# Kernel optimization log

Hardware: AMD Instinct MI355X
Metric: run time of the kernel (lower is better)

## Reference

```python
import jax, jax.numpy as jnp
import numpy as np

N_NODES = 50000


def _sage_conv(x, src, dst, Wl, Wr, b):
    """SAGEConv with mean aggregation: lin_l(mean_j x_j) + lin_r(x_i) + b."""
    msgs = x[src]                                                # [E, Din] gather
    agg = jax.ops.segment_sum(msgs, dst, num_segments=N_NODES)  # [N, Din] scatter-add
    cnt = jax.ops.segment_sum(jnp.ones((src.shape[0], 1), x.dtype), dst,
                              num_segments=N_NODES)             # [N, 1]
    agg = agg / jnp.maximum(cnt, 1.0)                           # mean
    return agg @ Wl.T + x @ Wr.T + b                            # [N, Dout]


def setup_inputs() -> dict:
    key = jax.random.key(0)
    ks = jax.random.split(key, 8)
    d_in, d_h = 64, 128
    x = jax.random.normal(ks[0], (N_NODES, d_in), dtype=jnp.float32)
    edge_index = jax.random.randint(ks[1], (2, 800000), 0, N_NODES, dtype=jnp.int32)
    s1 = 1.0 / np.sqrt(d_in)
    s2 = 1.0 / np.sqrt(d_h)
    return {
        "x": x,
        "edge_index": edge_index,
        "Wl1": jax.random.normal(ks[2], (d_h, d_in), dtype=jnp.float32) * s1,
        "Wr1": jax.random.normal(ks[3], (d_h, d_in), dtype=jnp.float32) * s1,
        "b1": jnp.zeros((d_h,), dtype=jnp.float32),
        "Wl2": jax.random.normal(ks[4], (d_h, d_h), dtype=jnp.float32) * s2,
        "Wr2": jax.random.normal(ks[5], (d_h, d_h), dtype=jnp.float32) * s2,
        "b2": jnp.zeros((d_h,), dtype=jnp.float32),
    }


def reference(x, edge_index, Wl1, Wr1, b1, Wl2, Wr2, b2):
    src, dst = edge_index[0], edge_index[1]
    # layer 1: conv -> dropout(eval: identity) -> ReLU
    h = jax.nn.relu(_sage_conv(x, src, dst, Wl1, Wr1, b1))
    # layer 2
    h = jax.nn.relu(_sage_conv(h, src, dst, Wl2, Wr2, b2))
    return h
```

## Files before the change

### kernel.cpp

```cpp
#include <hip/hip_runtime.h>

#define N_NODES 50000
#define NBUCK 391
#define BCAP 4096
#define BSHIFT 12

typedef __attribute__((ext_vector_type(8))) short short8;
typedef __attribute__((ext_vector_type(4))) float floatx4;

static __device__ __forceinline__ unsigned short f2bf(float f) {
  unsigned int u = __builtin_bit_cast(unsigned int, f);
  u += 0x7fff + ((u >> 16) & 1);
  return (unsigned short)(u >> 16);
}
static __device__ __forceinline__ float bf2f(unsigned short s) {
  unsigned int u = ((unsigned int)s) << 16;
  return __builtin_bit_cast(float, u);
}


__global__ void cast_x(const float* __restrict__ x, unsigned short* __restrict__ A1, int total) {
  int i = blockIdx.x * blockDim.x + threadIdx.x;
  if (i >= total) return;
  A1[(size_t)(i >> 6) * 128 + 64 + (i & 63)] = f2bf(x[i]);
}

__global__ void cast_w(const float* __restrict__ Wl1, const float* __restrict__ Wr1,
                       const float* __restrict__ Wl2, const float* __restrict__ Wr2,
                       unsigned short* __restrict__ W1, unsigned short* __restrict__ W2) {
  int t = blockIdx.x * blockDim.x + threadIdx.x;
  if (t < 128 * 128) {
    int c = t >> 7, k = t & 127;
    W1[t] = f2bf(k < 64 ? Wl1[c * 64 + k] : Wr1[c * 64 + k - 64]);
  } else {
    int t2 = t - 128 * 128;
    if (t2 < 128 * 256) {
      int c = t2 >> 8, k = t2 & 255;
      W2[t2] = f2bf(k < 128 ? Wl2[c * 128 + k] : Wr2[c * 128 + k - 128]);
    }
  }
}


__global__ void __launch_bounds__(1024) bucket_scatter(
    const int* __restrict__ src, const int* __restrict__ dst,
    int* __restrict__ bucket_cur, int* __restrict__ buf, int E) {
  __shared__ int hist[NBUCK];
  __shared__ int base_s[NBUCK];
  int t = threadIdx.x;
  for (int i = t; i < NBUCK; i += 1024) hist[i] = 0;
  __syncthreads();
  int e0 = blockIdx.x * 4096;
  int sv[4], dv[4], bv[4];
#pragma unroll
  for (int p = 0; p < 4; ++p) {
    int e = e0 + p * 1024 + t;
    if (e < E) {
      sv[p] = src[e];
      dv[p] = dst[e];
      bv[p] = dv[p] >> 7;
      atomicAdd(&hist[bv[p]], 1);
    } else bv[p] = -1;
  }
  __syncthreads();
  for (int i = t; i < NBUCK; i += 1024) {
    int c = hist[i];
    base_s[i] = c > 0 ? atomicAdd(&bucket_cur[i], c) : 0;
  }
  __syncthreads();
  for (int i = t; i < NBUCK; i += 1024) hist[i] = 0;
  __syncthreads();
#pragma unroll
  for (int p = 0; p < 4; ++p) {
    if (bv[p] >= 0) {
      int sub = base_s[bv[p]] + atomicAdd(&hist[bv[p]], 1);
      if (sub < BCAP) buf[(bv[p] << BSHIFT) + sub] = (sv[p] << 7) | (dv[p] & 127);
    }
  }
}

__global__ void __launch_bounds__(256) bucket_csr(
    int* __restrict__ buf, const int* __restrict__ bucket_cur,
    int* __restrict__ row_start, int* __restrict__ row_cnt, int n) {
  __shared__ int eb[BCAP];
  __shared__ int cnt[128];
  __shared__ int tmp[128];
  __shared__ int cur[128];
  const int t = threadIdx.x;
  const int b = blockIdx.x;
  const int node0 = b << 7;
  const int len = min(bucket_cur[b], BCAP);
  int* reg = buf + (b << BSHIFT);
  if (t < 128) cnt[t] = 0;
  __syncthreads();
  for (int i = t; i < len; i += 256) {
    int p = reg[i];
    eb[i] = p;
    atomicAdd(&cnt[p & 127], 1);
  }
  __syncthreads();
  if (t < 128) tmp[t] = cnt[t];
  __syncthreads();
#pragma unroll
  for (int off = 1; off < 128; off <<= 1) {
    int u = (t >= off && t < 128) ? tmp[t - off] : 0;
    __syncthreads();
    if (t < 128) tmp[t] += u;
    __syncthreads();
  }
  if (t < 128) {
    int ex = tmp[t] - cnt[t];
    cur[t] = ex;
    int nd = node0 + t;
    if (nd < n) {
      row_start[nd] = (b << BSHIFT) + ex;
      row_cnt[nd] = cnt[t];
    }
  }
  __syncthreads();
  for (int i = t; i < len; i += 256) {
    int p = eb[i];
    int sub = atomicAdd(&cur[p & 127], 1);
    reg[sub] = p >> 7;
  }
}


__global__ void agg_mean64(unsigned short* __restrict__ A1,
    const int* __restrict__ row_start, const int* __restrict__ row_cnt,
    const int* __restrict__ srcs, int n) {
  int wid = (blockIdx.x * blockDim.x + threadIdx.x) >> 6;
  int lane = threadIdx.x & 63;
  if (wid >= n) return;
  int start = row_start[wid];
  int cnt = row_cnt[wid];
  float a0 = 0.f, a1 = 0.f, a2 = 0.f, a3 = 0.f;
  int e = 0;
  for (; e + 4 <= cnt; e += 4) {
    int s0 = srcs[start + e];
    int s1 = srcs[start + e + 1];
    int s2 = srcs[start + e + 2];
    int s3 = srcs[start + e + 3];
    a0 += bf2f(A1[(size_t)s0 * 128 + 64 + lane]);
    a1 += bf2f(A1[(size_t)s1 * 128 + 64 + lane]);
    a2 += bf2f(A1[(size_t)s2 * 128 + 64 + lane]);
    a3 += bf2f(A1[(size_t)s3 * 128 + 64 + lane]);
  }
  for (; e < cnt; ++e) a0 += bf2f(A1[(size_t)srcs[start + e] * 128 + 64 + lane]);
  A1[(size_t)wid * 128 + lane] = f2bf((a0 + a1 + a2 + a3) * (1.0f / (float)max(cnt, 1)));
}

__global__ void agg_mean128(unsigned short* __restrict__ A2,
    const int* __restrict__ row_start, const int* __restrict__ row_cnt,
    const int* __restrict__ srcs, int n) {
  int wid = (blockIdx.x * blockDim.x + threadIdx.x) >> 6;
  int lane = threadIdx.x & 63;
  if (wid >= n) return;
  int start = row_start[wid];
  int cnt = row_cnt[wid];
  float ax = 0.f, ay = 0.f, bx = 0.f, by = 0.f;
  float cx = 0.f, cy = 0.f, dx = 0.f, dy = 0.f;
  int e = 0;
  for (; e + 4 <= cnt; e += 4) {
    int s0 = srcs[start + e];
    int s1 = srcs[start + e + 1];
    int s2 = srcs[start + e + 2];
    int s3 = srcs[start + e + 3];
    unsigned int u0 = *(const unsigned int*)(A2 + (size_t)s0 * 256 + 128 + lane * 2);
    unsigned int u1 = *(const unsigned int*)(A2 + (size_t)s1 * 256 + 128 + lane * 2);
    unsigned int u2 = *(const unsigned int*)(A2 + (size_t)s2 * 256 + 128 + lane * 2);
    unsigned int u3 = *(const unsigned int*)(A2 + (size_t)s3 * 256 + 128 + lane * 2);
    ax += bf2f((unsigned short)u0); ay += bf2f((unsigned short)(u0 >> 16));
    bx += bf2f((unsigned short)u1); by += bf2f((unsigned short)(u1 >> 16));
    cx += bf2f((unsigned short)u2); cy += bf2f((unsigned short)(u2 >> 16));
    dx += bf2f((unsigned short)u3); dy += bf2f((unsigned short)(u3 >> 16));
  }
  for (; e < cnt; ++e) {
    unsigned int u0 = *(const unsigned int*)(A2 + (size_t)srcs[start + e] * 256 + 128 + lane * 2);
    ax += bf2f((unsigned short)u0); ay += bf2f((unsigned short)(u0 >> 16));
  }
  float inv = 1.0f / (float)max(cnt, 1);
  unsigned int packed = (unsigned int)f2bf((ax + bx + cx + dx) * inv)
                      | ((unsigned int)f2bf((ay + by + cy + dy) * inv) << 16);
  *(unsigned int*)(A2 + (size_t)wid * 256 + lane * 2) = packed;
}


template<int KP, bool BF_OUT>
__global__ void __launch_bounds__(256) mfma_gemm(
    const unsigned short* __restrict__ A, const unsigned short* __restrict__ W,
    const float* __restrict__ bias, unsigned short* __restrict__ outb,
    float* __restrict__ outf, int n, int ostride, int ocol) {
  const int lane = threadIdx.x & 63;
  const int wv = threadIdx.x >> 6;
  const int m = lane & 15;
  const int q = lane >> 4;
  const int r0 = blockIdx.x * 128 + wv * 32;

  floatx4 acc[2][8];
#pragma unroll
  for (int rt = 0; rt < 2; ++rt)
#pragma unroll
    for (int ct = 0; ct < 8; ++ct) acc[rt][ct] = (floatx4){0.f, 0.f, 0.f, 0.f};

  int ra = r0 + m;      if (ra > n - 1) ra = n - 1;
  int rb = r0 + 16 + m; if (rb > n - 1) rb = n - 1;
  const unsigned short* Arow0 = A + (size_t)ra * KP + q * 8;
  const unsigned short* Arow1 = A + (size_t)rb * KP + q * 8;
  const unsigned short* Wrow  = W + (size_t)m * KP + q * 8;

#pragma unroll 1
  for (int kc = 0; kc < KP / 32; ++kc) {
    short8 a0 = *(const short8*)(Arow0 + kc * 32);
    short8 a1 = *(const short8*)(Arow1 + kc * 32);
#pragma unroll
    for (int ct = 0; ct < 8; ++ct) {
      short8 wf = *(const short8*)(Wrow + (size_t)ct * 16 * KP + kc * 32);
      acc[0][ct] = __builtin_amdgcn_mfma_f32_16x16x32_bf16(a0, wf, acc[0][ct], 0, 0, 0);
      acc[1][ct] = __builtin_amdgcn_mfma_f32_16x16x32_bf16(a1, wf, acc[1][ct], 0, 0, 0);
    }
  }

  float bv[8];
#pragma unroll
  for (int ct = 0; ct < 8; ++ct) bv[ct] = bias[ct * 16 + m];

#pragma unroll
  for (int rt = 0; rt < 2; ++rt) {
#pragma unroll
    for (int j = 0; j < 4; ++j) {
      int row = r0 + rt * 16 + q * 4 + j;
      if (row < n) {
#pragma unroll
        for (int ct = 0; ct < 8; ++ct) {
          float v = acc[rt][ct][j] + bv[ct];
          v = v > 0.f ? v : 0.f;
          int col = ct * 16 + m;
          if (BF_OUT) outb[(size_t)row * ostride + ocol + col] = f2bf(v);
          else        outf[(size_t)row * ostride + col] = v;
        }
      }
    }
  }
}


extern "C" void kernel_launch(void* const* d_in, const int* in_sizes, int n_in,
                              void* d_out, int out_size, void* d_ws, size_t ws_size,
                              hipStream_t stream) {
  const int N = N_NODES;
  const int E = in_sizes[1] / 2;
  const float* x   = (const float*)d_in[0];
  const int*   src = (const int*)d_in[1];
  const int*   dst = src + E;
  const float* Wl1 = (const float*)d_in[2];
  const float* Wr1 = (const float*)d_in[3];
  const float* b1  = (const float*)d_in[4];
  const float* Wl2 = (const float*)d_in[5];
  const float* Wr2 = (const float*)d_in[6];
  const float* b2  = (const float*)d_in[7];
  float* out = (float*)d_out;

  unsigned short* A1 = (unsigned short*)d_ws;
  unsigned short* A2 = A1 + (size_t)N * 128;
  unsigned short* W1 = A2 + (size_t)N * 256;
  unsigned short* W2 = W1 + 128 * 128;
  int* row_start  = (int*)(W2 + 128 * 256);
  int* row_cnt    = row_start + N;
  int* bucket_cur = row_cnt + N;
  int* buf        = bucket_cur + 392;

  hipMemsetAsync(bucket_cur, 0, NBUCK * sizeof(int), stream);
  cast_x<<<(N * 64 + 255) / 256, 256, 0, stream>>>(x, A1, N * 64);
  cast_w<<<(128 * 128 + 128 * 256 + 255) / 256, 256, 0, stream>>>(Wl1, Wr1, Wl2, Wr2, W1, W2);

  bucket_scatter<<<(E + 4095) / 4096, 1024, 0, stream>>>(src, dst, bucket_cur, buf, E);
  bucket_csr<<<NBUCK, 256, 0, stream>>>(buf, bucket_cur, row_start, row_cnt, N);

  int ab = (N * 64 + 255) / 256;
  agg_mean64<<<ab, 256, 0, stream>>>(A1, row_start, row_cnt, buf, N);

  int gb = (N + 127) / 128;
  mfma_gemm<128, true><<<gb, 256, 0, stream>>>(A1, W1, b1, A2, nullptr, N, 256, 128);

  agg_mean128<<<ab, 256, 0, stream>>>(A2, row_start, row_cnt, buf, N);
  mfma_gemm<256, false><<<gb, 256, 0, stream>>>(A2, W2, b2, nullptr, out, N, 128, 0);
}
```

Before: 215.3 us.

## Fuse prep casts and memset into one kernel; fuse CSR build with layer-1 aggregation

The x cast, weight casts and bucket counter memset are merged into a single grid-stride prep kernel, removing two launches and a memset. The per-bucket CSR builder now runs with 1024 threads and, after building its 128 node rows, does the layer-1 mean aggregation for those nodes directly from shared counts. This drops a separate aggregation launch and its row_start/row_cnt reads. The trade-off is lower parallelism: 391 blocks, each with 16 waves covering 128 nodes. The prep kernel also uses a fixed 512-block grid.

```diff
diff --git a/kernel.cpp b/kernel.cpp
--- a/kernel.cpp
+++ b/kernel.cpp
@@ -19,26 +19,25 @@
 }
 
 
-__global__ void cast_x(const float* __restrict__ x, unsigned short* __restrict__ A1, int total) {
-  int i = blockIdx.x * blockDim.x + threadIdx.x;
-  if (i >= total) return;
-  A1[(size_t)(i >> 6) * 128 + 64 + (i & 63)] = f2bf(x[i]);
-}
-
-__global__ void cast_w(const float* __restrict__ Wl1, const float* __restrict__ Wr1,
-                       const float* __restrict__ Wl2, const float* __restrict__ Wr2,
-                       unsigned short* __restrict__ W1, unsigned short* __restrict__ W2) {
-  int t = blockIdx.x * blockDim.x + threadIdx.x;
-  if (t < 128 * 128) {
-    int c = t >> 7, k = t & 127;
-    W1[t] = f2bf(k < 64 ? Wl1[c * 64 + k] : Wr1[c * 64 + k - 64]);
-  } else {
-    int t2 = t - 128 * 128;
-    if (t2 < 128 * 256) {
-      int c = t2 >> 8, k = t2 & 255;
-      W2[t2] = f2bf(k < 128 ? Wl2[c * 128 + k] : Wr2[c * 128 + k - 128]);
-    }
-  }
+__global__ void __launch_bounds__(256) prep(
+    const float* __restrict__ x,
+    const float* __restrict__ Wl1, const float* __restrict__ Wr1,
+    const float* __restrict__ Wl2, const float* __restrict__ Wr2,
+    unsigned short* __restrict__ A1, unsigned short* __restrict__ W1,
+    unsigned short* __restrict__ W2, int* __restrict__ bucket_cur, int n) {
+  const int gid = blockIdx.x * 256 + threadIdx.x;
+  const int gsz = gridDim.x * 256;
+  for (int i = gid; i < n * 64; i += gsz)
+    A1[(size_t)(i >> 6) * 128 + 64 + (i & 63)] = f2bf(x[i]);
+  for (int i = gid; i < 128 * 128; i += gsz) {
+    int c = i >> 7, k = i & 127;
+    W1[i] = f2bf(k < 64 ? Wl1[c * 64 + k] : Wr1[c * 64 + k - 64]);
+  }
+  for (int i = gid; i < 128 * 256; i += gsz) {
+    int c = i >> 8, k = i & 255;
+    W2[i] = f2bf(k < 128 ? Wl2[c * 128 + k] : Wr2[c * 128 + k - 128]);
+  }
+  for (int i = gid; i < NBUCK; i += gsz) bucket_cur[i] = 0;
 }
 
 
@@ -79,9 +78,11 @@
   }
 }
 
-__global__ void __launch_bounds__(256) bucket_csr(
+
+__global__ void __launch_bounds__(1024) bucket_csr_agg64(
     int* __restrict__ buf, const int* __restrict__ bucket_cur,
-    int* __restrict__ row_start, int* __restrict__ row_cnt, int n) {
+    int* __restrict__ row_start, int* __restrict__ row_cnt,
+    unsigned short* __restrict__ A1, int n) {
   __shared__ int eb[BCAP];
   __shared__ int cnt[128];
   __shared__ int tmp[128];
@@ -93,7 +94,7 @@
   int* reg = buf + (b << BSHIFT);
   if (t < 128) cnt[t] = 0;
   __syncthreads();
-  for (int i = t; i < len; i += 256) {
+  for (int i = t; i < len; i += 1024) {
     int p = reg[i];
     eb[i] = p;
     atomicAdd(&cnt[p & 127], 1);
@@ -118,37 +119,36 @@
     }
   }
   __syncthreads();
-  for (int i = t; i < len; i += 256) {
+  for (int i = t; i < len; i += 1024) {
     int p = eb[i];
     int sub = atomicAdd(&cur[p & 127], 1);
     reg[sub] = p >> 7;
   }
-}
-
-
-__global__ void agg_mean64(unsigned short* __restrict__ A1,
-    const int* __restrict__ row_start, const int* __restrict__ row_cnt,
-    const int* __restrict__ srcs, int n) {
-  int wid = (blockIdx.x * blockDim.x + threadIdx.x) >> 6;
-  int lane = threadIdx.x & 63;
-  if (wid >= n) return;
-  int start = row_start[wid];
-  int cnt = row_cnt[wid];
-  float a0 = 0.f, a1 = 0.f, a2 = 0.f, a3 = 0.f;
-  int e = 0;
-  for (; e + 4 <= cnt; e += 4) {
-    int s0 = srcs[start + e];
-    int s1 = srcs[start + e + 1];
-    int s2 = srcs[start + e + 2];
-    int s3 = srcs[start + e + 3];
-    a0 += bf2f(A1[(size_t)s0 * 128 + 64 + lane]);
-    a1 += bf2f(A1[(size_t)s1 * 128 + 64 + lane]);
-    a2 += bf2f(A1[(size_t)s2 * 128 + 64 + lane]);
-    a3 += bf2f(A1[(size_t)s3 * 128 + 64 + lane]);
-  }
-  for (; e < cnt; ++e) a0 += bf2f(A1[(size_t)srcs[start + e] * 128 + 64 + lane]);
-  A1[(size_t)wid * 128 + lane] = f2bf((a0 + a1 + a2 + a3) * (1.0f / (float)max(cnt, 1)));
-}
+  __syncthreads();
+  const int lane = t & 63;
+  const int wv = t >> 6;
+  for (int loc = wv; loc < 128; loc += 16) {
+    int nd = node0 + loc;
+    if (nd >= n) break;
+    int cn = cnt[loc];
+    const int* sp = reg + (tmp[loc] - cn);
+    float a0 = 0.f, a1 = 0.f, a2 = 0.f, a3 = 0.f;
+    int e = 0;
+    for (; e + 4 <= cn; e += 4) {
+      int s0 = sp[e];
+      int s1 = sp[e + 1];
+      int s2 = sp[e + 2];
+      int s3 = sp[e + 3];
+      a0 += bf2f(A1[(size_t)s0 * 128 + 64 + lane]);
+      a1 += bf2f(A1[(size_t)s1 * 128 + 64 + lane]);
+      a2 += bf2f(A1[(size_t)s2 * 128 + 64 + lane]);
+      a3 += bf2f(A1[(size_t)s3 * 128 + 64 + lane]);
+    }
+    for (; e < cn; ++e) a0 += bf2f(A1[(size_t)sp[e] * 128 + 64 + lane]);
+    A1[(size_t)nd * 128 + lane] = f2bf((a0 + a1 + a2 + a3) * (1.0f / (float)max(cn, 1)));
+  }
+}
+
 
 __global__ void agg_mean128(unsigned short* __restrict__ A2,
     const int* __restrict__ row_start, const int* __restrict__ row_cnt,
@@ -270,19 +270,14 @@
   int* bucket_cur = row_cnt + N;
   int* buf        = bucket_cur + 392;
 
-  hipMemsetAsync(bucket_cur, 0, NBUCK * sizeof(int), stream);
-  cast_x<<<(N * 64 + 255) / 256, 256, 0, stream>>>(x, A1, N * 64);
-  cast_w<<<(128 * 128 + 128 * 256 + 255) / 256, 256, 0, stream>>>(Wl1, Wr1, Wl2, Wr2, W1, W2);
-
+  prep<<<512, 256, 0, stream>>>(x, Wl1, Wr1, Wl2, Wr2, A1, W1, W2, bucket_cur, N);
   bucket_scatter<<<(E + 4095) / 4096, 1024, 0, stream>>>(src, dst, bucket_cur, buf, E);
-  bucket_csr<<<NBUCK, 256, 0, stream>>>(buf, bucket_cur, row_start, row_cnt, N);
-
-  int ab = (N * 64 + 255) / 256;
-  agg_mean64<<<ab, 256, 0, stream>>>(A1, row_start, row_cnt, buf, N);
+  bucket_csr_agg64<<<NBUCK, 1024, 0, stream>>>(buf, bucket_cur, row_start, row_cnt, A1, N);
 
   int gb = (N + 127) / 128;
   mfma_gemm<128, true><<<gb, 256, 0, stream>>>(A1, W1, b1, A2, nullptr, N, 256, 128);
 
+  int ab = (N * 64 + 255) / 256;
   agg_mean128<<<ab, 256, 0, stream>>>(A2, row_start, row_cnt, buf, N);
   mfma_gemm<256, false><<<gb, 256, 0, stream>>>(A2, W2, b2, nullptr, out, N, 128, 0);
 }
```

New measurement: 208.1 us. 3.3% less time.
